# Kernel tuning notes

Hardware: AMD Instinct MI355X
Metric: run time of the kernel (lower is better)

Reference implementation:

```python
import jax, jax.numpy as jnp
import numpy as np

DEPTH, DIM, HEADS, DIM_HEAD = 6, 1024, 16, 64
INNER = HEADS * DIM_HEAD  # 1024
DFF = 4 * DIM             # 4096
SCALE = DIM_HEAD ** -0.5


def setup_inputs() -> dict:
    key = jax.random.key(0)
    ks = jax.random.split(key, 12)
    def w(k, shape, fan_in):
        return jax.random.normal(k, shape, dtype=jnp.float32) * (fan_in ** -0.5)
    return {
        "x":     jax.random.normal(ks[0], (2, 2048, DIM), dtype=jnp.float32),
        "Wq":    w(ks[1], (DEPTH, DIM, INNER), DIM),
        "Wkv":   w(ks[2], (DEPTH, DIM, 2 * INNER), DIM),
        "Wo":    w(ks[3], (DEPTH, INNER, DIM), INNER),
        "bo":    jnp.zeros((DEPTH, DIM), dtype=jnp.float32),
        "ln1_g": jnp.ones((DEPTH, DIM), dtype=jnp.float32),
        "ln1_b": jnp.zeros((DEPTH, DIM), dtype=jnp.float32),
        "ln2_g": jnp.ones((DEPTH, DIM), dtype=jnp.float32),
        "ln2_b": jnp.zeros((DEPTH, DIM), dtype=jnp.float32),
        "W1":    w(ks[4], (DEPTH, DIM, DFF), DIM),
        "b1":    jnp.zeros((DEPTH, DFF), dtype=jnp.float32),
        "W2":    w(ks[5], (DEPTH, DFF, DIM), DFF),
        "b2":    jnp.zeros((DEPTH, DIM), dtype=jnp.float32),
    }


def _layernorm(x, g, b, eps=1e-5):
    mu = jnp.mean(x, axis=-1, keepdims=True)
    var = jnp.mean(jnp.square(x - mu), axis=-1, keepdims=True)
    return (x - mu) * jax.lax.rsqrt(var + eps) * g + b


def reference(x, Wq, Wkv, Wo, bo, ln1_g, ln1_b, ln2_g, ln2_b, W1, b1, W2, b2):
    b, n, _ = x.shape
    for l in range(DEPTH):
        # --- PreNorm self-attention ---
        h = _layernorm(x, ln1_g[l], ln1_b[l])
        q = h @ Wq[l]                       # [b, n, inner]
        kv = h @ Wkv[l]
        k, v = jnp.split(kv, 2, axis=-1)
        def heads(t):
            return t.reshape(b, n, HEADS, DIM_HEAD).transpose(0, 2, 1, 3)  # [b, h, n, d]
        q, k, v = heads(q), heads(k), heads(v)
        dots = jnp.einsum('bhid,bhjd->bhij', q, k) * SCALE
        attn = jax.nn.softmax(dots, axis=-1)
        out = jnp.einsum('bhij,bhjd->bhid', attn, v)
        out = out.transpose(0, 2, 1, 3).reshape(b, n, INNER)
        x = out @ Wo[l] + bo[l] + x
        # --- PreNorm feed-forward (exact GELU, matching torch nn.GELU default) ---
        h = _layernorm(x, ln2_g[l], ln2_b[l])
        h = jax.nn.gelu(h @ W1[l] + b1[l], approximate=False)
        x = h @ W2[l] + b2[l] + x
    return x
```

## Files before the change

kernel.cpp:

```cpp
#include <hip/hip_runtime.h>
#include <hip/hip_bf16.h>
#include <cstdint>
#include <cstddef>

#define DEPTH 6
#define DIM   1024
#define HEADS 16
#define DIMH  64
#define INNER 1024
#define DFF   4096
#define SEQ   2048
#define NTOK  4096

typedef __attribute__((ext_vector_type(8))) short bf16x8;
typedef __attribute__((ext_vector_type(4))) short bf16x4;
typedef __attribute__((ext_vector_type(4))) float f32x4;
typedef __hip_bfloat16 bf16;

#define CS 0.18033688011112042f
#define SMAX 24.0f

__device__ __forceinline__ void gld_lds16(const void* g, void* l) {
  __builtin_amdgcn_global_load_lds(
      (const __attribute__((address_space(1))) unsigned int*)g,
      (__attribute__((address_space(3))) unsigned int*)l,
      16, 0, 0);
}

__global__ __launch_bounds__(256) void transpose_convert(
    const float* __restrict__ in, bf16* __restrict__ out,
    int K, int N, int row0, int orows)
{
  __shared__ float tile[32][33];
  const int d  = blockIdx.z;
  const int n0 = blockIdx.x * 32, k0 = blockIdx.y * 32;
  const int c = threadIdx.x & 31, rb = threadIdx.x >> 5;
  const float* src = in + ((size_t)d * K + k0) * N + n0;
#pragma unroll
  for (int rr = 0; rr < 4; ++rr) {
    int r = rb + rr * 8;
    tile[r][c] = src[(size_t)r * N + c];
  }
  __syncthreads();
  bf16* dst = out + ((size_t)d * orows + row0 + n0) * K + k0;
#pragma unroll
  for (int rr = 0; rr < 4; ++rr) {
    int r = rb + rr * 8;
    dst[(size_t)r * K + c] = __float2bfloat16(tile[c][r]);
  }
}

__global__ __launch_bounds__(256) void ln_kernel(
    const float* __restrict__ x, const float* __restrict__ g,
    const float* __restrict__ b, bf16* __restrict__ h)
{
  const int row = blockIdx.x;
  const int tid = threadIdx.x;
  const float4 xv = *(const float4*)(x + (size_t)row * DIM + tid * 4);
  float s  = xv.x + xv.y + xv.z + xv.w;
  float s2 = xv.x * xv.x + xv.y * xv.y + xv.z * xv.z + xv.w * xv.w;
#pragma unroll
  for (int off = 1; off < 64; off <<= 1) {
    s  += __shfl_xor(s, off);
    s2 += __shfl_xor(s2, off);
  }
  __shared__ float red[8];
  const int wave = tid >> 6, lane = tid & 63;
  if (lane == 0) { red[wave * 2] = s; red[wave * 2 + 1] = s2; }
  __syncthreads();
  const float ts  = red[0] + red[2] + red[4] + red[6];
  const float ts2 = red[1] + red[3] + red[5] + red[7];
  const float mu  = ts * (1.0f / DIM);
  const float var = ts2 * (1.0f / DIM) - mu * mu;
  const float rstd = rsqrtf(var + 1e-5f);
  const float4 gv = *(const float4*)(g + tid * 4);
  const float4 bv = *(const float4*)(b + tid * 4);
  bf16 hv[4];
  hv[0] = __float2bfloat16((xv.x - mu) * rstd * gv.x + bv.x);
  hv[1] = __float2bfloat16((xv.y - mu) * rstd * gv.y + bv.y);
  hv[2] = __float2bfloat16((xv.z - mu) * rstd * gv.z + bv.z);
  hv[3] = __float2bfloat16((xv.w - mu) * rstd * gv.w + bv.w);
  *(uint2*)(h + (size_t)row * DIM + tid * 4) = *(uint2*)hv;
}

template<int EPI, bool SWZ, int BN, int BK>
__global__ __launch_bounds__(512, 4) void gemm_t(
    const bf16* __restrict__ A, const bf16* __restrict__ Bt,
    int N, int K,
    const float* __restrict__ bias,
    float* __restrict__ outf, bf16* __restrict__ outb,
    bf16* __restrict__ outq, bf16* __restrict__ outk, bf16* __restrict__ outvt)
{
  constexpr int NW = BN / 32;
  constexpr int CH = BK / 8;
  constexpr int CM = CH - 1;
  constexpr int RB = BK * 2;
  constexpr int RPG = 512 / CH;
  constexpr int NA = 128 / RPG;
  constexpr int NB = BN / RPG;
  __shared__ alignas(16) bf16 As[128 * BK];
  __shared__ alignas(16) bf16 Bs[BN * BK];
  const int tid  = threadIdx.x;
  const int lane = tid & 63;
  const int wave = tid >> 6;
  const int wr = wave >> 1;
  const int wc = wave & 1;

  int bx, by;
  if (SWZ) {
    const int gx   = (int)gridDim.x;
    const int nwg  = gx * (int)gridDim.y;
    const int wg   = blockIdx.x + blockIdx.y * gx;
    const int xcd  = wg & 7;
    const int slot = wg >> 3;
    const int id   = xcd * (nwg >> 3) + slot;
    by = id / gx;
    bx = id % gx;
  } else {
    bx = blockIdx.x; by = blockIdx.y;
  }
  const int m0 = by * 128, n0 = bx * BN;
  const int sr = tid / CH, pc = tid % CH;
  const int lc = pc ^ (sr & CM);

  f32x4 acc[2][NW];
#pragma unroll
  for (int m = 0; m < 2; ++m)
#pragma unroll
    for (int n = 0; n < NW; ++n) acc[m][n] = (f32x4){0.f, 0.f, 0.f, 0.f};

  for (int k0 = 0; k0 < K; k0 += BK) {
#pragma unroll
    for (int it = 0; it < NA; ++it)
      gld_lds16(A + (size_t)(m0 + it * RPG + sr) * K + k0 + lc * 8,
                (char*)As + it * 8192 + tid * 16);
#pragma unroll
    for (int it = 0; it < NB; ++it)
      gld_lds16(Bt + (size_t)(n0 + it * RPG + sr) * K + k0 + lc * 8,
                (char*)Bs + it * 8192 + tid * 16);
    __syncthreads();
#pragma unroll
    for (int kk = 0; kk < BK / 32; ++kk) {
      const int cb = kk * 4 + (lane >> 4);
      bf16x8 af[2], bfr[NW];
#pragma unroll
      for (int m = 0; m < 2; ++m) {
        const int r = wr * 32 + m * 16 + (lane & 15);
        af[m] = *(const bf16x8*)((const char*)As + r * RB + ((cb ^ (r & CM)) << 4));
      }
#pragma unroll
      for (int n = 0; n < NW; ++n) {
        const int r = wc * (BN / 2) + n * 16 + (lane & 15);
        bfr[n] = *(const bf16x8*)((const char*)Bs + r * RB + ((cb ^ (r & CM)) << 4));
      }
#pragma unroll
      for (int m = 0; m < 2; ++m)
#pragma unroll
        for (int n = 0; n < NW; ++n)
          acc[m][n] = __builtin_amdgcn_mfma_f32_16x16x32_bf16(af[m], bfr[n], acc[m][n], 0, 0, 0);
    }
    __syncthreads();
  }

#pragma unroll
  for (int m = 0; m < 2; ++m) {
    const int rb = m0 + wr * 32 + m * 16 + ((lane >> 4) << 2);
#pragma unroll
    for (int n = 0; n < NW; ++n) {
      const int col = n0 + wc * (BN / 2) + n * 16 + (lane & 15);
      if (EPI == 0 && col >= 2048) {
        const int batch = rb >> 11, tok = rb & 2047;
        const int c = col - 2048;
        union { bf16x4 v4; short s[4]; } w;
#pragma unroll
        for (int j = 0; j < 4; ++j) {
          const bf16 bb = __float2bfloat16(acc[m][n][j]);
          w.s[j] = *(const short*)&bb;
        }
        *(bf16x4*)(outvt + (((size_t)(batch * HEADS + (c >> 6))) * DIMH + (c & 63)) * SEQ + tok)
            = w.v4;
        continue;
      }
#pragma unroll
      for (int j = 0; j < 4; ++j) {
        const int row = rb + j;
        const float v = acc[m][n][j];
        if (EPI == 0) {
          const int batch = row >> 11, tok = row & 2047;
          if (col < 1024) {
            outq[(((size_t)(batch * HEADS + (col >> 6))) * SEQ + tok) * DIMH + (col & 63)] =
                __float2bfloat16(v * CS);
          } else {
            const int c = col - 1024;
            outk[(((size_t)(batch * HEADS + (c >> 6))) * SEQ + tok) * DIMH + (c & 63)] =
                __float2bfloat16(v);
          }
        } else if (EPI == 1) {
          const size_t off = (size_t)row * N + col;
          outf[off] = v + bias[col] + outf[off];
        } else if (EPI == 2) {
          const float t = v + bias[col];
          const float gg = 0.5f * t * (1.0f + erff(t * 0.70710678118654752f));
          outb[(size_t)row * N + col] = __float2bfloat16(gg);
        }
      }
    }
  }
}

__global__ __launch_bounds__(512) void attn_kernel(
    const bf16* __restrict__ q, const bf16* __restrict__ k,
    const bf16* __restrict__ vt, bf16* __restrict__ out)
{
  __shared__ alignas(16) bf16 Ks[2][2][64 * 64];
  __shared__ alignas(16) bf16 Vs[2][2][64 * 64];
  const int tid  = threadIdx.x;
  const int lane = tid & 63;
  const int wave = tid >> 6;
  const int g    = lane >> 4;
  const int lm   = lane & 15;

  const int gx   = (int)gridDim.x;
  const int nwg  = gx * (int)gridDim.y;
  const int wg   = blockIdx.x + blockIdx.y * gx;
  const int id   = (wg & 7) * (nwg >> 3) + (wg >> 3);
  const int bh   = id / gx;
  const int qw   = (id % gx) * 128 + wave * 16;

  const int sr = tid >> 3, pc = tid & 7;

  bf16x8 qf[2];
#pragma unroll
  for (int kk = 0; kk < 2; ++kk)
    qf[kk] = *(const bf16x8*)(q + ((size_t)bh * SEQ + qw + lm) * DIMH + kk * 32 + g * 8);

  union { bf16x8 v8; short s[8]; } ones_u;
#pragma unroll
  for (int i = 0; i < 8; ++i) ones_u.s[i] = 0x3F80;
  const bf16x8 onesA = ones_u.v8;

  f32x4 ao[4];
#pragma unroll
  for (int n = 0; n < 4; ++n) ao[n] = (f32x4){0.f, 0.f, 0.f, 0.f};
  f32x4 lsum = (f32x4){0.f, 0.f, 0.f, 0.f};

  const int lc = pc ^ (sr & 7);
  auto stage = [&](int jt2, int buf) {
#pragma unroll
    for (int sub = 0; sub < 2; ++sub) {
      const int jt = jt2 * 2 + sub;
      gld_lds16(k  + ((size_t)bh * SEQ + jt * 64 + sr) * DIMH + lc * 8,
                (char*)&Ks[buf][sub][0] + tid * 16);
      gld_lds16(vt + ((size_t)bh * DIMH + sr) * SEQ + jt * 64 + lc * 8,
                (char*)&Vs[buf][sub][0] + tid * 16);
    }
  };

  stage(0, 0);

  for (int jt2 = 0; jt2 < SEQ / 128; ++jt2) {
    const int buf = jt2 & 1;
    const bool pref = (jt2 + 1 < SEQ / 128);
    if (pref) {
      stage(jt2 + 1, buf ^ 1);
      asm volatile("s_waitcnt vmcnt(4)" ::: "memory");
    } else {
      asm volatile("s_waitcnt vmcnt(0)" ::: "memory");
    }
    __builtin_amdgcn_s_barrier();

#pragma unroll
    for (int sub = 0; sub < 2; ++sub) {
      f32x4 sa[4];
#pragma unroll
      for (int n = 0; n < 4; ++n)
        sa[n] = (f32x4){-SMAX, -SMAX, -SMAX, -SMAX};
      __builtin_amdgcn_s_setprio(1);
#pragma unroll
      for (int kk = 0; kk < 2; ++kk)
#pragma unroll
        for (int n = 0; n < 4; ++n) {
          const int row = n * 16 + lm;
          const bf16x8 af = *(const bf16x8*)((const char*)&Ks[buf][sub][0] + row * 128
                                             + (((kk * 4 + g) ^ (row & 7)) << 4));
          sa[n] = __builtin_amdgcn_mfma_f32_16x16x32_bf16(af, qf[kk], sa[n], 0, 0, 0);
        }
      __builtin_amdgcn_s_setprio(0);

      bf16x8 pa[2];
#pragma unroll
      for (int n = 0; n < 4; ++n)
#pragma unroll
        for (int r = 0; r < 4; ++r)
          sa[n][r] = exp2f(sa[n][r]);
#pragma unroll
      for (int h = 0; h < 2; ++h) {
        union { bf16x8 v8; short s[8]; } u;
#pragma unroll
        for (int n2 = 0; n2 < 2; ++n2)
#pragma unroll
          for (int r = 0; r < 4; ++r) {
            const bf16 bb = __float2bfloat16(sa[h * 2 + n2][r]);
            u.s[n2 * 4 + r] = *(const short*)&bb;
          }
        pa[h] = u.v8;
      }

      __builtin_amdgcn_s_setprio(1);
#pragma unroll
      for (int kk = 0; kk < 2; ++kk)
        lsum = __builtin_amdgcn_mfma_f32_16x16x32_bf16(onesA, pa[kk], lsum, 0, 0, 0);
#pragma unroll
      for (int n = 0; n < 4; ++n) {
        const int row = n * 16 + lm;
        const char* vb = (const char*)&Vs[buf][sub][0] + row * 128;
        const int sw = row & 7;
#pragma unroll
        for (int kk = 0; kk < 2; ++kk) {
          const bf16x4 lo = *(const bf16x4*)(vb + (((kk * 4 + (g >> 1)) ^ sw) << 4) + (g & 1) * 8);
          const bf16x4 hi = *(const bf16x4*)(vb + (((kk * 4 + 2 + (g >> 1)) ^ sw) << 4) + (g & 1) * 8);
          const bf16x8 vf = __builtin_shufflevector(lo, hi, 0, 1, 2, 3, 4, 5, 6, 7);
          ao[n] = __builtin_amdgcn_mfma_f32_16x16x32_bf16(vf, pa[kk], ao[n], 0, 0, 0);
        }
      }
      __builtin_amdgcn_s_setprio(0);
    }
    __builtin_amdgcn_s_barrier();
  }

  const int batch = bh >> 4, head = bh & 15;
  const float linv = 1.0f / lsum[0];
  const int row = qw + lm;
  bf16* orow = out + ((size_t)batch * SEQ + row) * INNER + head * DIMH;
#pragma unroll
  for (int n = 0; n < 4; ++n) {
    union { bf16x4 v4; short s[4]; } w;
#pragma unroll
    for (int r = 0; r < 4; ++r) {
      const bf16 bb = __float2bfloat16(ao[n][r] * linv);
      w.s[r] = *(const short*)&bb;
    }
    *(bf16x4*)(orow + n * 16 + g * 4) = w.v4;
  }
}

extern "C" void kernel_launch(void* const* d_in, const int* in_sizes, int n_in,
                              void* d_out, int out_size, void* d_ws, size_t ws_size,
                              hipStream_t stream)
{
  (void)in_sizes; (void)n_in; (void)out_size; (void)ws_size;
  const float* x_in = (const float*)d_in[0];
  const float* Wq   = (const float*)d_in[1];
  const float* Wkv  = (const float*)d_in[2];
  const float* Wo   = (const float*)d_in[3];
  const float* bo   = (const float*)d_in[4];
  const float* ln1g = (const float*)d_in[5];
  const float* ln1b = (const float*)d_in[6];
  const float* ln2g = (const float*)d_in[7];
  const float* ln2b = (const float*)d_in[8];
  const float* W1   = (const float*)d_in[9];
  const float* b1   = (const float*)d_in[10];
  const float* W2   = (const float*)d_in[11];
  const float* b2   = (const float*)d_in[12];
  float* xb = (float*)d_out;

  char* ws = (char*)d_ws;
  size_t off = 0;
  auto take = [&](size_t bytes) {
    char* p = ws + off;
    off += (bytes + 255) & ~(size_t)255;
    return p;
  };
  bf16* Wqkvt = (bf16*)take((size_t)DEPTH * 3072 * 1024 * 2);
  bf16* Wot   = (bf16*)take((size_t)DEPTH * 1024 * 1024 * 2);
  bf16* W1t   = (bf16*)take((size_t)DEPTH * 4096 * 1024 * 2);
  bf16* W2t   = (bf16*)take((size_t)DEPTH * 1024 * 4096 * 2);
  bf16* hb    = (bf16*)take((size_t)NTOK * DIM * 2);
  bf16* qbuf  = (bf16*)take((size_t)NTOK * INNER * 2);
  bf16* kbuf  = (bf16*)take((size_t)NTOK * INNER * 2);
  bf16* vtbuf = (bf16*)take((size_t)NTOK * INNER * 2);
  bf16* aobuf = (bf16*)take((size_t)NTOK * INNER * 2);
  bf16* h1buf = (bf16*)take((size_t)NTOK * DFF * 2);

  hipMemcpyAsync(xb, x_in, (size_t)NTOK * DIM * 4, hipMemcpyDeviceToDevice, stream);

  dim3 b256(256);
  dim3 b512(512);
  transpose_convert<<<dim3(32, 32, DEPTH),  b256, 0, stream>>>(Wq,  Wqkvt, 1024, 1024, 0,    3072);
  transpose_convert<<<dim3(64, 32, DEPTH),  b256, 0, stream>>>(Wkv, Wqkvt, 1024, 2048, 1024, 3072);
  transpose_convert<<<dim3(32, 32, DEPTH),  b256, 0, stream>>>(Wo,  Wot,   1024, 1024, 0,    1024);
  transpose_convert<<<dim3(128, 32, DEPTH), b256, 0, stream>>>(W1,  W1t,   1024, 4096, 0,    4096);
  transpose_convert<<<dim3(32, 128, DEPTH), b256, 0, stream>>>(W2,  W2t,   4096, 1024, 0,    1024);

  for (int l = 0; l < DEPTH; ++l) {
    ln_kernel<<<NTOK, b256, 0, stream>>>(xb, ln1g + l * DIM, ln1b + l * DIM, hb);
    gemm_t<0, true, 128, 64><<<dim3(3072 / 128, NTOK / 128), b512, 0, stream>>>(
        hb, Wqkvt + (size_t)l * 3072 * 1024, 3072, 1024,
        nullptr, nullptr, nullptr, qbuf, kbuf, vtbuf);
    attn_kernel<<<dim3(SEQ / 128, 32), b512, 0, stream>>>(qbuf, kbuf, vtbuf, aobuf);
    gemm_t<1, true, 64, 128><<<dim3(1024 / 64, NTOK / 128), b512, 0, stream>>>(
        aobuf, Wot + (size_t)l * 1024 * 1024, 1024, 1024,
        bo + l * DIM, xb, nullptr, nullptr, nullptr, nullptr);
    ln_kernel<<<NTOK, b256, 0, stream>>>(xb, ln2g + l * DIM, ln2b + l * DIM, hb);
    gemm_t<2, true, 128, 64><<<dim3(4096 / 128, NTOK / 128), b512, 0, stream>>>(
        hb, W1t + (size_t)l * 4096 * 1024, 4096, 1024,
        b1 + l * DFF, nullptr, h1buf, nullptr, nullptr, nullptr);
    gemm_t<1, true, 64, 128><<<dim3(1024 / 64, NTOK / 128), b512, 0, stream>>>(
        h1buf, W2t + (size_t)l * 1024 * 4096, 1024, 4096,
        b2 + l * DIM, xb, nullptr, nullptr, nullptr, nullptr);
  }
}
```

Before: 1.445 ms.

## Double-buffer LDS tiles in residual-output GEMMs to overlap loads with MFMA

Adds a templated double-buffering mode to the GEMM kernel. The next K tile is issued to the alternate LDS buffer while the current tile is being computed, and one barrier per iteration is dropped. The two GEMMs that write into the residual stream (Wo and W2) switch to this mode with BK reduced from 128 to 64, which keeps LDS use the same. The goal is to hide global-to-LDS latency. The cost is twice as many K iterations and barriers, and it relies on the async LDS loads being complete by the time of the following barrier.

```diff
diff --git a/kernel.cpp b/kernel.cpp
--- a/kernel.cpp
+++ b/kernel.cpp
@@ -83,7 +83,7 @@
   *(uint2*)(h + (size_t)row * DIM + tid * 4) = *(uint2*)hv;
 }
 
-template<int EPI, bool SWZ, int BN, int BK>
+template<int EPI, bool SWZ, int BN, int BK, bool DBUF>
 __global__ __launch_bounds__(512, 4) void gemm_t(
     const bf16* __restrict__ A, const bf16* __restrict__ Bt,
     int N, int K,
@@ -98,8 +98,9 @@
   constexpr int RPG = 512 / CH;
   constexpr int NA = 128 / RPG;
   constexpr int NB = BN / RPG;
-  __shared__ alignas(16) bf16 As[128 * BK];
-  __shared__ alignas(16) bf16 Bs[BN * BK];
+  constexpr int NBUF = DBUF ? 2 : 1;
+  __shared__ alignas(16) bf16 As[NBUF][128 * BK];
+  __shared__ alignas(16) bf16 Bs[NBUF][BN * BK];
   const int tid  = threadIdx.x;
   const int lane = tid & 63;
   const int wave = tid >> 6;
@@ -129,16 +130,18 @@
 #pragma unroll
     for (int n = 0; n < NW; ++n) acc[m][n] = (f32x4){0.f, 0.f, 0.f, 0.f};
 
-  for (int k0 = 0; k0 < K; k0 += BK) {
+  auto stage = [&](int k0, int b) {
 #pragma unroll
     for (int it = 0; it < NA; ++it)
       gld_lds16(A + (size_t)(m0 + it * RPG + sr) * K + k0 + lc * 8,
-                (char*)As + it * 8192 + tid * 16);
+                (char*)&As[b][0] + it * 8192 + tid * 16);
 #pragma unroll
     for (int it = 0; it < NB; ++it)
       gld_lds16(Bt + (size_t)(n0 + it * RPG + sr) * K + k0 + lc * 8,
-                (char*)Bs + it * 8192 + tid * 16);
-    __syncthreads();
+                (char*)&Bs[b][0] + it * 8192 + tid * 16);
+  };
+
+  auto compute = [&](int b) {
 #pragma unroll
     for (int kk = 0; kk < BK / 32; ++kk) {
       const int cb = kk * 4 + (lane >> 4);
@@ -146,12 +149,12 @@
 #pragma unroll
       for (int m = 0; m < 2; ++m) {
         const int r = wr * 32 + m * 16 + (lane & 15);
-        af[m] = *(const bf16x8*)((const char*)As + r * RB + ((cb ^ (r & CM)) << 4));
+        af[m] = *(const bf16x8*)((const char*)&As[b][0] + r * RB + ((cb ^ (r & CM)) << 4));
       }
 #pragma unroll
       for (int n = 0; n < NW; ++n) {
         const int r = wc * (BN / 2) + n * 16 + (lane & 15);
-        bfr[n] = *(const bf16x8*)((const char*)Bs + r * RB + ((cb ^ (r & CM)) << 4));
+        bfr[n] = *(const bf16x8*)((const char*)&Bs[b][0] + r * RB + ((cb ^ (r & CM)) << 4));
       }
 #pragma unroll
       for (int m = 0; m < 2; ++m)
@@ -159,7 +162,24 @@
         for (int n = 0; n < NW; ++n)
           acc[m][n] = __builtin_amdgcn_mfma_f32_16x16x32_bf16(af[m], bfr[n], acc[m][n], 0, 0, 0);
     }
+  };
+
+  if (DBUF) {
+    const int nt = K / BK;
+    stage(0, 0);
     __syncthreads();
+    for (int t = 0; t < nt; ++t) {
+      if (t + 1 < nt) stage((t + 1) * BK, (t + 1) & 1);
+      compute(t & 1);
+      __syncthreads();
+    }
+  } else {
+    for (int k0 = 0; k0 < K; k0 += BK) {
+      stage(k0, 0);
+      __syncthreads();
+      compute(0);
+      __syncthreads();
+    }
   }
 
 #pragma unroll
@@ -394,18 +414,18 @@
 
   for (int l = 0; l < DEPTH; ++l) {
     ln_kernel<<<NTOK, b256, 0, stream>>>(xb, ln1g + l * DIM, ln1b + l * DIM, hb);
-    gemm_t<0, true, 128, 64><<<dim3(3072 / 128, NTOK / 128), b512, 0, stream>>>(
+    gemm_t<0, true, 128, 64, false><<<dim3(3072 / 128, NTOK / 128), b512, 0, stream>>>(
         hb, Wqkvt + (size_t)l * 3072 * 1024, 3072, 1024,
         nullptr, nullptr, nullptr, qbuf, kbuf, vtbuf);
     attn_kernel<<<dim3(SEQ / 128, 32), b512, 0, stream>>>(qbuf, kbuf, vtbuf, aobuf);
-    gemm_t<1, true, 64, 128><<<dim3(1024 / 64, NTOK / 128), b512, 0, stream>>>(
+    gemm_t<1, true, 64, 64, true><<<dim3(1024 / 64, NTOK / 128), b512, 0, stream>>>(
         aobuf, Wot + (size_t)l * 1024 * 1024, 1024, 1024,
         bo + l * DIM, xb, nullptr, nullptr, nullptr, nullptr);
     ln_kernel<<<NTOK, b256, 0, stream>>>(xb, ln2g + l * DIM, ln2b + l * DIM, hb);
-    gemm_t<2, true, 128, 64><<<dim3(4096 / 128, NTOK / 128), b512, 0, stream>>>(
+    gemm_t<2, true, 128, 64, false><<<dim3(4096 / 128, NTOK / 128), b512, 0, stream>>>(
         hb, W1t + (size_t)l * 4096 * 1024, 4096, 1024,
         b1 + l * DFF, nullptr, h1buf, nullptr, nullptr, nullptr);
-    gemm_t<1, true, 64, 128><<<dim3(1024 / 64, NTOK / 128), b512, 0, stream>>>(
+    gemm_t<1, true, 64, 64, true><<<dim3(1024 / 64, NTOK / 128), b512, 0, stream>>>(
         h1buf, W2t + (size_t)l * 1024 * 4096, 1024, 4096,
         b2 + l * DIM, xb, nullptr, nullptr, nullptr, nullptr);
   }
```

New measurement: 1.502 ms. 4.0% more time.
